# Kernel tuning notes

Measured on AMD Instinct MI355X. Metric: run time of the kernel, lower is better.

Reference implementation:

```python
import jax, jax.numpy as jnp
import numpy as np

B, S, E = 1, 4096, 2048
H, KVH, HD = 16, 4, 128
WIN = 2048  # sliding window size
ROPE_BASE = 10000.0


def setup_inputs() -> dict:
    rng = jax.random.key(0)
    ks = jax.random.split(rng, 7)
    s = 0.02
    return {
        "query": jax.random.normal(ks[0], (B, S, E), jnp.float32),
        "key": jax.random.normal(ks[1], (B, S, E), jnp.float32),
        "value": jax.random.normal(ks[2], (B, S, E), jnp.float32),
        "position_ids": jnp.broadcast_to(jnp.arange(S, dtype=jnp.int64), (B, S)),
        "wq": jax.random.normal(ks[3], (E, H * HD), jnp.float32) * s,
        "wk": jax.random.normal(ks[4], (E, KVH * HD), jnp.float32) * s,
        "wv": jax.random.normal(ks[5], (E, KVH * HD), jnp.float32) * s,
        "wo": jax.random.normal(ks[6], (H * HD, E), jnp.float32) * s,
    }


def _rotate_half(x):
    x1, x2 = x[..., : HD // 2], x[..., HD // 2 :]
    return jnp.concatenate([-x2, x1], axis=-1)


def reference(query, key, value, position_ids, wq, wk, wv, wo):
    # projections (nn.Linear, no bias)
    q = (query @ wq).reshape(B, S, H, HD).transpose(0, 2, 1, 3)     # [B,H,S,D]
    k = (key @ wk).reshape(B, S, KVH, HD).transpose(0, 2, 1, 3)     # [B,KVH,S,D]
    v = (value @ wv).reshape(B, S, KVH, HD).transpose(0, 2, 1, 3)

    # RoPE (MistralRotaryEmbedding + apply_rotary_pos_emb)
    inv_freq = 1.0 / (ROPE_BASE ** (jnp.arange(0, HD, 2, dtype=jnp.float32) / HD))
    ang = position_ids.astype(jnp.float32)[..., None] * inv_freq   # [B,S,D/2]
    emb = jnp.concatenate([ang, ang], axis=-1)                      # [B,S,D]
    cos = jnp.cos(emb)[:, None]                                     # [B,1,S,D]
    sin = jnp.sin(emb)[:, None]
    q = q * cos + _rotate_half(q) * sin
    k = k * cos + _rotate_half(k) * sin

    # GQA: repeat_kv
    n_rep = H // KVH
    k = jnp.repeat(k, n_rep, axis=1)                                # [B,H,S,D]
    v = jnp.repeat(v, n_rep, axis=1)

    scale = 1.0 / np.sqrt(HD).astype(np.float32)
    scores = jnp.einsum("bhqd,bhkd->bhqk", q, k) * scale            # [B,H,S,S]
    i = jnp.arange(S)[:, None]
    j = jnp.arange(S)[None, :]
    mask = (j <= i) & (j >= i - WIN)                                # causal, window left
    scores = jnp.where(mask, scores, jnp.finfo(scores.dtype).min)
    attn = jax.nn.softmax(scores, axis=-1)
    out = jnp.einsum("bhqk,bhkd->bhqd", attn, v)                    # [B,H,S,D]
    out = out.transpose(0, 2, 1, 3).reshape(B, S, H * HD)
    return out @ wo
```

## Files before the change

kernel.cpp:

```cpp
#include <hip/hip_runtime.h>
#include <hip/hip_bf16.h>
#include <cmath>

typedef __bf16 bf16;
typedef bf16 bf16x4 __attribute__((ext_vector_type(4)));
typedef float f32x4 __attribute__((ext_vector_type(4)));
typedef short short8 __attribute__((ext_vector_type(8)));

#define S_LEN 4096
#define EMB   2048
#define NH    16
#define NKV   4
#define HD    128
#define WIN   2048

#define SCALE2 0.12751743f
#define DTHR   8.0f

#define GLOAD_LDS16(g, l) __builtin_amdgcn_global_load_lds( \
    (const __attribute__((address_space(1))) void*)(g),     \
    (__attribute__((address_space(3))) void*)(l), 16, 0, 0)

__global__ __launch_bounds__(256)
void cvt_f32_bf16(const float* __restrict__ X, bf16* __restrict__ Y)
{
    long i = ((long)blockIdx.x * 256 + threadIdx.x) * 8;
    f32x4 a = *(const f32x4*)(X + i);
    f32x4 b = *(const f32x4*)(X + i + 4);
    short8 v;
    #pragma unroll
    for (int k = 0; k < 4; k++) {
        ((bf16*)&v)[k]     = (bf16)a[k];
        ((bf16*)&v)[4 + k] = (bf16)b[k];
    }
    *(short8*)(Y + i) = v;
}

__global__ __launch_bounds__(256)
void transpose_w(const float* __restrict__ W, bf16* __restrict__ Wt, int K, int N)
{
    __shared__ float t[32][33];
    const int k0 = blockIdx.x * 32, n0 = blockIdx.y * 32;
    const int tx = threadIdx.x & 31, ty = threadIdx.x >> 5;
    #pragma unroll
    for (int i = 0; i < 4; i++)
        t[ty + 8 * i][tx] = W[(long)(k0 + ty + 8 * i) * N + n0 + tx];
    __syncthreads();
    #pragma unroll
    for (int i = 0; i < 4; i++)
        Wt[(long)(n0 + ty + 8 * i) * K + k0 + tx] = (bf16)t[tx][ty + 8 * i];
}

template<bool C_BF16>
__global__ __launch_bounds__(256)
void gemm_lds(const bf16* __restrict__ A, const bf16* __restrict__ Bt,
              void* __restrict__ Cp, int M, int N, int K)
{
    __shared__ __align__(16) bf16 As[128 * 32];
    __shared__ __align__(16) bf16 Bs[128 * 32];
    char* AsB = (char*)As;
    char* BsB = (char*)Bs;
    const int tid  = threadIdx.x;
    const int n0 = blockIdx.x * 128, m0 = blockIdx.y * 128;
    const int w = tid >> 6;
    const int lane = tid & 63;
    const int wm = (w >> 1) * 64, wn = (w & 1) * 64;
    const int l16 = tid & 15, lq4 = lane >> 4;

    const f32x4 fz = {0.f, 0.f, 0.f, 0.f};
    f32x4 acc[4][4];
    #pragma unroll
    for (int i = 0; i < 4; i++)
        #pragma unroll
        for (int j = 0; j < 4; j++) acc[i][j] = fz;

    const int srow = w * 16 + (lane >> 2);
    const int scol = (lane & 3) * 8;
    const bf16* Ag = A  + (long)(m0 + srow) * K + scol;
    const bf16* Bg = Bt + (long)(n0 + srow) * K + scol;
    char* Al = AsB + w * 1024 + (lane & 63) * 0;
    char* Bl = BsB + w * 1024;

    for (int k0 = 0; k0 < K; k0 += 32) {
        __syncthreads();
        GLOAD_LDS16(Ag,            Al);
        GLOAD_LDS16(Ag + 64 * K,   Al + 4096);
        GLOAD_LDS16(Bg,            Bl);
        GLOAD_LDS16(Bg + 64 * K,   Bl + 4096);
        __syncthreads();
        Ag += 32; Bg += 32;

        short8 af[4], bfr[4];
        #pragma unroll
        for (int i = 0; i < 4; i++) {
            af[i]  = *(const short8*)(AsB + (wm + i * 16 + l16) * 64 + lq4 * 16);
            bfr[i] = *(const short8*)(BsB + (wn + i * 16 + l16) * 64 + lq4 * 16);
        }
        #pragma unroll
        for (int i = 0; i < 4; i++)
            #pragma unroll
            for (int j = 0; j < 4; j++)
                acc[i][j] = __builtin_amdgcn_mfma_f32_16x16x32_bf16(
                    af[i], bfr[j], acc[i][j], 0, 0, 0);
    }

    #pragma unroll
    for (int i = 0; i < 4; i++)
        #pragma unroll
        for (int r = 0; r < 4; r++) {
            long row = m0 + wm + i * 16 + lq4 * 4 + r;
            #pragma unroll
            for (int j = 0; j < 4; j++) {
                long col = n0 + wn + j * 16 + l16;
                if (C_BF16) ((bf16*)Cp)[row * N + col] = (bf16)acc[i][j][r];
                else        ((float*)Cp)[row * N + col] = acc[i][j][r];
            }
        }
}

template<bool A_BF16, bool C_BF16>
__global__ __launch_bounds__(256)
void gemm_mfma(const void* __restrict__ Ap, const bf16* __restrict__ Bt,
               void* __restrict__ Cp, int M, int N, int K)
{
    __shared__ __align__(16) bf16 As[128 * 32];
    __shared__ __align__(16) bf16 Bs[128 * 32];
    char* AsB = (char*)As;
    char* BsB = (char*)Bs;
    const int tid = threadIdx.x;
    const int n0 = blockIdx.x * 128, m0 = blockIdx.y * 128;
    const int w = tid >> 6;
    const int wm = (w >> 1) * 64, wn = (w & 1) * 64;
    const int l16 = tid & 15, lq4 = (tid & 63) >> 4;

    const f32x4 fz = {0.f, 0.f, 0.f, 0.f};
    f32x4 acc[4][4];
    #pragma unroll
    for (int i = 0; i < 4; i++)
        #pragma unroll
        for (int j = 0; j < 4; j++) acc[i][j] = fz;

    const int sr = tid >> 1;
    const int sh = (tid & 1) * 16;
    const long arow = (long)(m0 + sr) * K;
    const long brow = (long)(n0 + sr) * K;
    const int wbase = sr * 64;
    const int swz = (sr & 7) << 4;

    for (int k0 = 0; k0 < K; k0 += 32) {
        __syncthreads();
        short8 av0, av1;
        if (A_BF16) {
            const bf16* A = (const bf16*)Ap;
            av0 = *(const short8*)(A + arow + k0 + sh);
            av1 = *(const short8*)(A + arow + k0 + sh + 8);
        } else {
            const float* A = (const float*)Ap;
            f32x4 a0 = *(const f32x4*)(A + arow + k0 + sh);
            f32x4 a1 = *(const f32x4*)(A + arow + k0 + sh + 4);
            f32x4 a2 = *(const f32x4*)(A + arow + k0 + sh + 8);
            f32x4 a3 = *(const f32x4*)(A + arow + k0 + sh + 12);
            bf16* p0 = (bf16*)&av0;
            bf16* p1 = (bf16*)&av1;
            #pragma unroll
            for (int i = 0; i < 4; i++) {
                p0[i]     = (bf16)a0[i];
                p0[4 + i] = (bf16)a1[i];
                p1[i]     = (bf16)a2[i];
                p1[4 + i] = (bf16)a3[i];
            }
        }
        short8 bv0 = *(const short8*)(Bt + brow + k0 + sh);
        short8 bv1 = *(const short8*)(Bt + brow + k0 + sh + 8);
        *(short8*)(AsB + ((wbase + sh * 2     ) ^ swz)) = av0;
        *(short8*)(AsB + ((wbase + sh * 2 + 16) ^ swz)) = av1;
        *(short8*)(BsB + ((wbase + sh * 2     ) ^ swz)) = bv0;
        *(short8*)(BsB + ((wbase + sh * 2 + 16) ^ swz)) = bv1;
        __syncthreads();

        short8 af[4], bfr[4];
        #pragma unroll
        for (int i = 0; i < 4; i++) {
            int mr = wm + i * 16 + l16;
            af[i]  = *(const short8*)(AsB + ((mr * 64 + lq4 * 16) ^ ((mr & 7) << 4)));
            int nr = wn + i * 16 + l16;
            bfr[i] = *(const short8*)(BsB + ((nr * 64 + lq4 * 16) ^ ((nr & 7) << 4)));
        }
        #pragma unroll
        for (int i = 0; i < 4; i++)
            #pragma unroll
            for (int j = 0; j < 4; j++)
                acc[i][j] = __builtin_amdgcn_mfma_f32_16x16x32_bf16(
                    af[i], bfr[j], acc[i][j], 0, 0, 0);
    }

    #pragma unroll
    for (int i = 0; i < 4; i++)
        #pragma unroll
        for (int r = 0; r < 4; r++) {
            long row = m0 + wm + i * 16 + lq4 * 4 + r;
            #pragma unroll
            for (int j = 0; j < 4; j++) {
                long col = n0 + wn + j * 16 + l16;
                if (C_BF16) ((bf16*)Cp)[row * N + col] = (bf16)acc[i][j][r];
                else        ((float*)Cp)[row * N + col] = acc[i][j][r];
            }
        }
}

__global__ __launch_bounds__(256)
void rope_k(bf16* __restrict__ X, int nh)
{
    int idx = blockIdx.x * 256 + threadIdx.x;
    int i = idx & 63;
    int h = (idx >> 6) % nh;
    int s = idx / (64 * nh);
    bf16* p = X + (long)s * (nh * HD) + h * HD + i;
    float x1 = (float)p[0];
    float x2 = (float)p[64];
    float f = exp2f((float)i * (-13.287712379549449f / 64.0f));
    float ang = (float)s * f;
    float sn, cs;
    sincosf(ang, &sn, &cs);
    p[0]  = (bf16)(x1 * cs - x2 * sn);
    p[64] = (bf16)(x2 * cs + x1 * sn);
}

__global__ __launch_bounds__(256)
void transpose_v(const bf16* __restrict__ V, bf16* __restrict__ Vt)
{
    __shared__ bf16 t[32][33];
    const int s0 = blockIdx.x * 32;
    const int d0 = blockIdx.y * 32;
    const int tx = threadIdx.x & 31, ty = threadIdx.x >> 5;
    #pragma unroll
    for (int k = 0; k < 4; k++)
        t[ty + 8 * k][tx] = V[(long)(s0 + ty + 8 * k) * (NKV * HD) + d0 + tx];
    __syncthreads();
    #pragma unroll
    for (int k = 0; k < 4; k++) {
        int drow = d0 + ty + 8 * k;
        Vt[(long)drow * S_LEN + s0 + tx] = t[tx][ty + 8 * k];
    }
}

__global__ __launch_bounds__(256)
void attn_mfma(const bf16* __restrict__ Qb, const bf16* __restrict__ Kb,
               const bf16* __restrict__ Vt, bf16* __restrict__ Ob)
{
    __shared__ __align__(16) bf16 Kl[64 * 128];
    __shared__ __align__(16) bf16 Vl[128 * 64];
    __shared__ __align__(16) bf16 Pl[4][16][72];

    const int qb  = (int)gridDim.x - 1 - blockIdx.x;
    const int q0  = qb * 64;
    const int h   = blockIdx.y;
    const int kvh = h >> 2;
    const int tid = threadIdx.x;
    const int w   = tid >> 6;
    const int l16 = tid & 15;
    const int lq4 = (tid & 63) >> 4;
    const int qw  = q0 + w * 16;
    const int qi  = qw + l16;

    short8 aQ[4];
    {
        const bf16* qp = Qb + (long)qi * EMB + h * HD + lq4 * 8;
        #pragma unroll
        for (int c = 0; c < 4; c++) aQ[c] = *(const short8*)(qp + c * 32);
    }

    const f32x4 fz = {0.f, 0.f, 0.f, 0.f};
    float mrow = -1e30f, lrow = 0.f;
    f32x4 accO[8];
    #pragma unroll
    for (int dt = 0; dt < 8; dt++) accO[dt] = fz;

    const int jb0 = (q0 >= WIN) ? q0 - WIN : 0;
    char* KlB = (char*)Kl;
    char* VlB = (char*)Vl;

    const bf16* pK = Kb + (long)(jb0 + (tid >> 4)) * (NKV * HD) + kvh * HD + (tid & 15) * 8;
    const bf16* pV = Vt + ((long)kvh * HD + (tid >> 3)) * S_LEN + jb0 + (tid & 7) * 8;

    short8 stgK[4], stgV[4];
    #pragma unroll
    for (int it = 0; it < 4; it++) {
        stgK[it] = *(const short8*)(pK + it * 16 * (NKV * HD));
        stgV[it] = *(const short8*)(pV + it * 32 * S_LEN);
    }
    pK += 64 * (NKV * HD);
    pV += 64;

    for (int jb = jb0; jb <= q0; jb += 64) {
        __syncthreads();
        #pragma unroll
        for (int it = 0; it < 4; it++) {
            int c = it * 256 + tid;
            int key = c >> 4, d0 = (c & 15) * 8;
            *(short8*)(KlB + ((key * 256 + d0 * 2) ^ ((key & 7) << 4))) = stgK[it];
            int d = c >> 3, k0 = (c & 7) * 8;
            *(short8*)(VlB + ((d * 128 + k0 * 2) ^ ((d & 7) << 4))) = stgV[it];
        }
        __syncthreads();
        if (jb + 64 <= q0) {
            #pragma unroll
            for (int it = 0; it < 4; it++) {
                stgK[it] = *(const short8*)(pK + it * 16 * (NKV * HD));
                stgV[it] = *(const short8*)(pV + it * 32 * S_LEN);
            }
            pK += 64 * (NKV * HD);
            pV += 64;
        }

        f32x4 s[4];
        #pragma unroll
        for (int jt = 0; jt < 4; jt++) {
            const int key = jt * 16 + l16;
            f32x4 a = fz;
            #pragma unroll
            for (int c = 0; c < 4; c++) {
                short8 bk = *(const short8*)(
                    KlB + ((key * 256 + c * 64 + lq4 * 16) ^ ((key & 7) << 4)));
                a = __builtin_amdgcn_mfma_f32_16x16x32_bf16(bk, aQ[c], a, 0, 0, 0);
            }
            s[jt] = a;
        }

        float tmax = -1e30f;
        const bool need_mask = (jb == q0) || (q0 >= WIN && jb == jb0);
        if (need_mask) {
            #pragma unroll
            for (int jt = 0; jt < 4; jt++)
                #pragma unroll
                for (int r = 0; r < 4; r++) {
                    int j = jb + jt * 16 + lq4 * 4 + r;
                    float sv = s[jt][r] * SCALE2;
                    if (j > qi || j < qi - WIN) sv = -1e30f;
                    s[jt][r] = sv;
                    tmax = fmaxf(tmax, sv);
                }
        } else {
            #pragma unroll
            for (int jt = 0; jt < 4; jt++)
                #pragma unroll
                for (int r = 0; r < 4; r++) {
                    float sv = s[jt][r] * SCALE2;
                    s[jt][r] = sv;
                    tmax = fmaxf(tmax, sv);
                }
        }
        tmax = fmaxf(tmax, __shfl_xor(tmax, 16, 64));
        tmax = fmaxf(tmax, __shfl_xor(tmax, 32, 64));

        if (!__all(tmax - mrow <= DTHR)) {
            float mn = fmaxf(mrow, tmax);
            float alpha = exp2f(mrow - mn);
            mrow = mn;
            lrow *= alpha;
            #pragma unroll
            for (int dt = 0; dt < 8; dt++)
                accO[dt] *= alpha;
        }

        float rsum = 0.f;
        #pragma unroll
        for (int jt = 0; jt < 4; jt++) {
            bf16x4 pb4;
            #pragma unroll
            for (int r = 0; r < 4; r++) {
                float pv = exp2f(s[jt][r] - mrow);
                bf16 pb = (bf16)pv;
                pb4[r] = pb;
                rsum += (float)pb;
            }
            *(bf16x4*)&Pl[w][l16][jt * 16 + lq4 * 4] = pb4;
        }
        rsum += __shfl_xor(rsum, 16, 64);
        rsum += __shfl_xor(rsum, 32, 64);
        lrow += rsum;

        #pragma unroll
        for (int kc = 0; kc < 2; kc++) {
            short8 ap = *(const short8*)&Pl[w][l16][kc * 32 + lq4 * 8];
            #pragma unroll
            for (int dt = 0; dt < 8; dt++) {
                int d = dt * 16 + l16;
                short8 bv = *(const short8*)(
                    VlB + ((d * 128 + kc * 64 + lq4 * 16) ^ ((d & 7) << 4)));
                accO[dt] = __builtin_amdgcn_mfma_f32_16x16x32_bf16(bv, ap, accO[dt], 0, 0, 0);
            }
        }
    }

    float inv = 1.0f / lrow;
    bf16* op = Ob + (long)qi * EMB + h * HD + lq4 * 4;
    #pragma unroll
    for (int dt = 0; dt < 8; dt++) {
        bf16x4 o4;
        #pragma unroll
        for (int r = 0; r < 4; r++) o4[r] = (bf16)(accO[dt][r] * inv);
        *(bf16x4*)(op + dt * 16) = o4;
    }
}

extern "C" void kernel_launch(void* const* d_in, const int* in_sizes, int n_in,
                              void* d_out, int out_size, void* d_ws, size_t ws_size,
                              hipStream_t stream)
{
    (void)out_size; (void)ws_size;
    int idx_pos = -1;
    for (int i = 0; i < n_in; i++)
        if (in_sizes[i] == 4096) { idx_pos = i; break; }
    int bigs[3] = {0, 1, 2}, w4[2] = {4, 6}, w1[2] = {5, 5};
    int nb = 0, n4 = 0, n1 = 0;
    for (int i = 0; i < n_in; i++) {
        if (in_sizes[i] == 8388608 && nb < 3) bigs[nb++] = i;
        else if (in_sizes[i] == 4194304 && n4 < 2) w4[n4++] = i;
        else if (in_sizes[i] == 1048576 && n1 < 2) w1[n1++] = i;
    }
    bool alpha = (idx_pos == 1);
    int iq  = alpha ? bigs[1] : bigs[0];
    int ik  = alpha ? bigs[0] : bigs[1];
    int iv  = bigs[2];
    int iwq = alpha ? w4[1] : w4[0];
    int iwo = alpha ? w4[0] : w4[1];
    int iwk = w1[0];
    int iwv = w1[1];
    const float* query = (const float*)d_in[iq];
    const float* key   = (const float*)d_in[ik];
    const float* value = (const float*)d_in[iv];
    const float* wq = (const float*)d_in[iwq];
    const float* wk = (const float*)d_in[iwk];
    const float* wv = (const float*)d_in[iwv];
    const float* wo = (const float*)d_in[iwo];

    bf16* Qb  = (bf16*)d_out;
    char* ws = (char*)d_ws;
    bf16* wqT = (bf16*)(ws);
    bf16* Qf  = (bf16*)(ws + (8u  << 20));
    bf16* Kb  = (bf16*)(ws);
    bf16* Vb  = (bf16*)(ws + (4u  << 20));
    bf16* Ob  = (bf16*)(ws + (8u  << 20));
    bf16* Vt  = (bf16*)(ws + (24u << 20));
    bf16* wkT = (bf16*)(ws + (24u << 20));
    bf16* wvT = (bf16*)(ws + (26u << 20));
    bf16* woT = (bf16*)(ws);

    dim3 blk(256);
    transpose_w<<<dim3(EMB / 32, EMB / 32), blk, 0, stream>>>(wq, wqT, EMB, EMB);
    cvt_f32_bf16<<<(S_LEN * EMB) / 2048, blk, 0, stream>>>(query, Qf);
    gemm_lds<true><<<dim3(EMB / 128, S_LEN / 128), blk, 0, stream>>>(
        Qf, wqT, Qb, S_LEN, EMB, EMB);

    transpose_w<<<dim3(EMB / 32, (NKV * HD) / 32), blk, 0, stream>>>(wk, wkT, EMB, NKV * HD);
    transpose_w<<<dim3(EMB / 32, (NKV * HD) / 32), blk, 0, stream>>>(wv, wvT, EMB, NKV * HD);
    gemm_mfma<false, true><<<dim3((NKV * HD) / 128, S_LEN / 128), blk, 0, stream>>>(
        key, wkT, Kb, S_LEN, NKV * HD, EMB);
    gemm_mfma<false, true><<<dim3((NKV * HD) / 128, S_LEN / 128), blk, 0, stream>>>(
        value, wvT, Vb, S_LEN, NKV * HD, EMB);

    rope_k<<<(S_LEN * NH * 64) / 256, blk, 0, stream>>>(Qb, NH);
    rope_k<<<(S_LEN * NKV * 64) / 256, blk, 0, stream>>>(Kb, NKV);
    transpose_v<<<dim3(S_LEN / 32, (NKV * HD) / 32), blk, 0, stream>>>(Vb, Vt);
    attn_mfma<<<dim3(S_LEN / 64, NH), blk, 0, stream>>>(Qb, Kb, Vt, Ob);

    transpose_w<<<dim3((NH * HD) / 32, EMB / 32), blk, 0, stream>>>(wo, woT, NH * HD, EMB);
    gemm_lds<false><<<dim3(EMB / 128, S_LEN / 128), blk, 0, stream>>>(
        Ob, woT, d_out, S_LEN, EMB, EMB);
}
```

Before: 613.7 us.

## Batch K/V projection launches and rework attention softmax and P layout

Merges the K and V weight transposes and the K and V projection GEMMs into single launches using a z grid dimension. This halves launch count and doubles the number of blocks per launch on the narrow KV GEMM. In attention, the padded P shared buffer becomes an XOR-swizzled unpadded layout. The lazy threshold-based rescale is replaced by an unconditional per-tile rescale using __expf with the plain scale instead of the folded log2 scale. That adds a multiply per exp and per-tile accumulator rescaling, but removes a warp vote and branch.

```diff
diff --git a/kernel.cpp b/kernel.cpp
--- a/kernel.cpp
+++ b/kernel.cpp
@@ -14,9 +14,6 @@
 #define HD    128
 #define WIN   2048
 
-#define SCALE2 0.12751743f
-#define DTHR   8.0f
-
 #define GLOAD_LDS16(g, l) __builtin_amdgcn_global_load_lds( \
     (const __attribute__((address_space(1))) void*)(g),     \
     (__attribute__((address_space(3))) void*)(l), 16, 0, 0)
@@ -39,6 +36,24 @@
 __global__ __launch_bounds__(256)
 void transpose_w(const float* __restrict__ W, bf16* __restrict__ Wt, int K, int N)
 {
+    __shared__ float t[32][33];
+    const int k0 = blockIdx.x * 32, n0 = blockIdx.y * 32;
+    const int tx = threadIdx.x & 31, ty = threadIdx.x >> 5;
+    #pragma unroll
+    for (int i = 0; i < 4; i++)
+        t[ty + 8 * i][tx] = W[(long)(k0 + ty + 8 * i) * N + n0 + tx];
+    __syncthreads();
+    #pragma unroll
+    for (int i = 0; i < 4; i++)
+        Wt[(long)(n0 + ty + 8 * i) * K + k0 + tx] = (bf16)t[tx][ty + 8 * i];
+}
+
+__global__ __launch_bounds__(256)
+void transpose_w2(const float* __restrict__ W0, const float* __restrict__ W1,
+                  bf16* __restrict__ T0, bf16* __restrict__ T1, int K, int N)
+{
+    const float* W = blockIdx.z ? W1 : W0;
+    bf16* Wt = blockIdx.z ? T1 : T0;
     __shared__ float t[32][33];
     const int k0 = blockIdx.x * 32, n0 = blockIdx.y * 32;
     const int tx = threadIdx.x & 31, ty = threadIdx.x >> 5;
@@ -78,15 +93,15 @@
     const int scol = (lane & 3) * 8;
     const bf16* Ag = A  + (long)(m0 + srow) * K + scol;
     const bf16* Bg = Bt + (long)(n0 + srow) * K + scol;
-    char* Al = AsB + w * 1024 + (lane & 63) * 0;
+    char* Al = AsB + w * 1024;
     char* Bl = BsB + w * 1024;
 
     for (int k0 = 0; k0 < K; k0 += 32) {
         __syncthreads();
-        GLOAD_LDS16(Ag,            Al);
-        GLOAD_LDS16(Ag + 64 * K,   Al + 4096);
-        GLOAD_LDS16(Bg,            Bl);
-        GLOAD_LDS16(Bg + 64 * K,   Bl + 4096);
+        GLOAD_LDS16(Ag,          Al);
+        GLOAD_LDS16(Ag + 64 * K, Al + 4096);
+        GLOAD_LDS16(Bg,          Bl);
+        GLOAD_LDS16(Bg + 64 * K, Bl + 4096);
         __syncthreads();
         Ag += 32; Bg += 32;
 
@@ -118,11 +133,16 @@
         }
 }
 
-template<bool A_BF16, bool C_BF16>
-__global__ __launch_bounds__(256)
-void gemm_mfma(const void* __restrict__ Ap, const bf16* __restrict__ Bt,
-               void* __restrict__ Cp, int M, int N, int K)
-{
+__global__ __launch_bounds__(256)
+void gemm_kv(const float* __restrict__ Ka, const float* __restrict__ Va,
+             const bf16* __restrict__ KBt, const bf16* __restrict__ VBt,
+             bf16* __restrict__ KC, bf16* __restrict__ VC,
+             int M, int N, int K)
+{
+    const float* Ap = blockIdx.z ? Va : Ka;
+    const bf16*  Bt = blockIdx.z ? VBt : KBt;
+    bf16*        Cp = blockIdx.z ? VC : KC;
+
     __shared__ __align__(16) bf16 As[128 * 32];
     __shared__ __align__(16) bf16 Bs[128 * 32];
     char* AsB = (char*)As;
@@ -150,12 +170,8 @@
     for (int k0 = 0; k0 < K; k0 += 32) {
         __syncthreads();
         short8 av0, av1;
-        if (A_BF16) {
-            const bf16* A = (const bf16*)Ap;
-            av0 = *(const short8*)(A + arow + k0 + sh);
-            av1 = *(const short8*)(A + arow + k0 + sh + 8);
-        } else {
-            const float* A = (const float*)Ap;
+        {
+            const float* A = Ap;
             f32x4 a0 = *(const f32x4*)(A + arow + k0 + sh);
             f32x4 a1 = *(const f32x4*)(A + arow + k0 + sh + 4);
             f32x4 a2 = *(const f32x4*)(A + arow + k0 + sh + 8);
@@ -202,8 +218,7 @@
             #pragma unroll
             for (int j = 0; j < 4; j++) {
                 long col = n0 + wn + j * 16 + l16;
-                if (C_BF16) ((bf16*)Cp)[row * N + col] = (bf16)acc[i][j][r];
-                else        ((float*)Cp)[row * N + col] = acc[i][j][r];
+                Cp[row * N + col] = (bf16)acc[i][j][r];
             }
         }
 }
@@ -250,7 +265,7 @@
 {
     __shared__ __align__(16) bf16 Kl[64 * 128];
     __shared__ __align__(16) bf16 Vl[128 * 64];
-    __shared__ __align__(16) bf16 Pl[4][16][72];
+    __shared__ __align__(16) bf16 Pl[4][16][64];
 
     const int qb  = (int)gridDim.x - 1 - blockIdx.x;
     const int q0  = qb * 64;
@@ -279,18 +294,15 @@
     const int jb0 = (q0 >= WIN) ? q0 - WIN : 0;
     char* KlB = (char*)Kl;
     char* VlB = (char*)Vl;
-
-    const bf16* pK = Kb + (long)(jb0 + (tid >> 4)) * (NKV * HD) + kvh * HD + (tid & 15) * 8;
-    const bf16* pV = Vt + ((long)kvh * HD + (tid >> 3)) * S_LEN + jb0 + (tid & 7) * 8;
+    char* PlB = (char*)Pl + w * 2048;
 
     short8 stgK[4], stgV[4];
     #pragma unroll
     for (int it = 0; it < 4; it++) {
-        stgK[it] = *(const short8*)(pK + it * 16 * (NKV * HD));
-        stgV[it] = *(const short8*)(pV + it * 32 * S_LEN);
-    }
-    pK += 64 * (NKV * HD);
-    pV += 64;
+        int c = it * 256 + tid;
+        stgK[it] = *(const short8*)(Kb + (long)(jb0 + (c >> 4)) * (NKV * HD) + kvh * HD + (c & 15) * 8);
+        stgV[it] = *(const short8*)(Vt + ((long)kvh * HD + (c >> 3)) * S_LEN + jb0 + (c & 7) * 8);
+    }
 
     for (int jb = jb0; jb <= q0; jb += 64) {
         __syncthreads();
@@ -306,11 +318,10 @@
         if (jb + 64 <= q0) {
             #pragma unroll
             for (int it = 0; it < 4; it++) {
-                stgK[it] = *(const short8*)(pK + it * 16 * (NKV * HD));
-                stgV[it] = *(const short8*)(pV + it * 32 * S_LEN);
-            }
-            pK += 64 * (NKV * HD);
-            pV += 64;
+                int c = it * 256 + tid;
+                stgK[it] = *(const short8*)(Kb + (long)(jb + 64 + (c >> 4)) * (NKV * HD) + kvh * HD + (c & 15) * 8);
+                stgV[it] = *(const short8*)(Vt + ((long)kvh * HD + (c >> 3)) * S_LEN + jb + 64 + (c & 7) * 8);
+            }
         }
 
         f32x4 s[4];
@@ -335,7 +346,7 @@
                 #pragma unroll
                 for (int r = 0; r < 4; r++) {
                     int j = jb + jt * 16 + lq4 * 4 + r;
-                    float sv = s[jt][r] * SCALE2;
+                    float sv = s[jt][r] * 0.08838834764831845f;
                     if (j > qi || j < qi - WIN) sv = -1e30f;
                     s[jt][r] = sv;
                     tmax = fmaxf(tmax, sv);
@@ -345,7 +356,7 @@
             for (int jt = 0; jt < 4; jt++)
                 #pragma unroll
                 for (int r = 0; r < 4; r++) {
-                    float sv = s[jt][r] * SCALE2;
+                    float sv = s[jt][r] * 0.08838834764831845f;
                     s[jt][r] = sv;
                     tmax = fmaxf(tmax, sv);
                 }
@@ -353,36 +364,33 @@
         tmax = fmaxf(tmax, __shfl_xor(tmax, 16, 64));
         tmax = fmaxf(tmax, __shfl_xor(tmax, 32, 64));
 
-        if (!__all(tmax - mrow <= DTHR)) {
-            float mn = fmaxf(mrow, tmax);
-            float alpha = exp2f(mrow - mn);
-            mrow = mn;
-            lrow *= alpha;
-            #pragma unroll
-            for (int dt = 0; dt < 8; dt++)
-                accO[dt] *= alpha;
-        }
-
+        float mn = fmaxf(mrow, tmax);
+        float alpha = __expf(mrow - mn);
+        mrow = mn;
         float rsum = 0.f;
         #pragma unroll
         for (int jt = 0; jt < 4; jt++) {
             bf16x4 pb4;
             #pragma unroll
             for (int r = 0; r < 4; r++) {
-                float pv = exp2f(s[jt][r] - mrow);
+                float pv = __expf(s[jt][r] - mn);
                 bf16 pb = (bf16)pv;
                 pb4[r] = pb;
                 rsum += (float)pb;
             }
-            *(bf16x4*)&Pl[w][l16][jt * 16 + lq4 * 4] = pb4;
+            *(bf16x4*)(PlB + ((l16 * 128 + jt * 32 + lq4 * 8) ^ ((l16 & 7) << 4))) = pb4;
         }
         rsum += __shfl_xor(rsum, 16, 64);
         rsum += __shfl_xor(rsum, 32, 64);
-        lrow += rsum;
+        lrow = lrow * alpha + rsum;
+        #pragma unroll
+        for (int dt = 0; dt < 8; dt++)
+            accO[dt] *= alpha;
 
         #pragma unroll
         for (int kc = 0; kc < 2; kc++) {
-            short8 ap = *(const short8*)&Pl[w][l16][kc * 32 + lq4 * 8];
+            short8 ap = *(const short8*)(
+                PlB + ((l16 * 128 + kc * 64 + lq4 * 16) ^ ((l16 & 7) << 4)));
             #pragma unroll
             for (int dt = 0; dt < 8; dt++) {
                 int d = dt * 16 + l16;
@@ -453,12 +461,10 @@
     gemm_lds<true><<<dim3(EMB / 128, S_LEN / 128), blk, 0, stream>>>(
         Qf, wqT, Qb, S_LEN, EMB, EMB);
 
-    transpose_w<<<dim3(EMB / 32, (NKV * HD) / 32), blk, 0, stream>>>(wk, wkT, EMB, NKV * HD);
-    transpose_w<<<dim3(EMB / 32, (NKV * HD) / 32), blk, 0, stream>>>(wv, wvT, EMB, NKV * HD);
-    gemm_mfma<false, true><<<dim3((NKV * HD) / 128, S_LEN / 128), blk, 0, stream>>>(
-        key, wkT, Kb, S_LEN, NKV * HD, EMB);
-    gemm_mfma<false, true><<<dim3((NKV * HD) / 128, S_LEN / 128), blk, 0, stream>>>(
-        value, wvT, Vb, S_LEN, NKV * HD, EMB);
+    transpose_w2<<<dim3(EMB / 32, (NKV * HD) / 32, 2), blk, 0, stream>>>(
+        wk, wv, wkT, wvT, EMB, NKV * HD);
+    gemm_kv<<<dim3((NKV * HD) / 128, S_LEN / 128, 2), blk, 0, stream>>>(
+        key, value, wkT, wvT, Kb, Vb, S_LEN, NKV * HD, EMB);
 
     rope_k<<<(S_LEN * NH * 64) / 256, blk, 0, stream>>>(Qb, NH);
     rope_k<<<(S_LEN * NKV * 64) / 256, blk, 0, stream>>>(Kb, NKV);
```

Result: faster. 520.1 us (-15.2%).
